# Optimization experiments

Hardware: AMD Instinct MI355X
Metric: run time of the kernel (lower is better)

## Reference

```python
import jax, jax.numpy as jnp
import numpy as np

B, L, D = 4, 2048, 1024
H, DK, DV = 16, 64, 64
TEMP = 8.0  # sqrt(DK)


def setup_inputs() -> dict:
    key = jax.random.key(0)
    ks = jax.random.split(key, 10)
    s = 0.02
    return {
        "q": jax.random.normal(ks[0], (B, L, D), jnp.float32),
        "k": jax.random.normal(ks[1], (B, L, D), jnp.float32),
        "v": jax.random.normal(ks[2], (B, L, D), jnp.float32),
        "mask": jax.random.randint(ks[3], (B, L, L), 0, 2).astype(jnp.int32),
        "Wq": jax.random.normal(ks[4], (D, H * DK), jnp.float32) * s,
        "bq": jnp.zeros((H * DK,), jnp.float32),
        "Wk": jax.random.normal(ks[5], (D, H * DK), jnp.float32) * s,
        "bk": jnp.zeros((H * DK,), jnp.float32),
        "Wv": jax.random.normal(ks[6], (D, H * DV), jnp.float32) * s,
        "bv": jnp.zeros((H * DV,), jnp.float32),
        "Wfc": jax.random.normal(ks[7], (H * DV, D), jnp.float32) * s,
        "bfc": jnp.zeros((D,), jnp.float32),
    }


def reference(q, k, v, mask, Wq, bq, Wk, bk, Wv, bv, Wfc, bfc):
    Bq, Lq, _ = q.shape
    res = q
    # QKV projections -> [B, H, L, dk/dv]
    qh = (q @ Wq + bq).reshape(Bq, Lq, H, DK).swapaxes(1, 2)
    kh = (k @ Wk + bk).reshape(Bq, k.shape[1], H, DK).swapaxes(1, 2)
    vh = (v @ Wv + bv).reshape(Bq, v.shape[1], H, DV).swapaxes(1, 2)
    # scaled scores [B, H, Lq, Lk]
    att = jnp.einsum("bhqd,bhkd->bhqk", qh / TEMP, kh)
    att = jnp.where(mask[:, None, :, :] == 0, jnp.float32(-1e9), att)
    att = jax.nn.softmax(att, axis=-1)
    # attend -> [B, H, Lq, dv] -> [B, Lq, H*dv]
    out = jnp.einsum("bhqk,bhkd->bhqd", att, vh)
    out = out.swapaxes(1, 2).reshape(Bq, Lq, H * DV)
    out = out @ Wfc + bfc + res  # dropout is identity in eval mode
    return (out, att)
```

## Files before the change

### kernel.cpp

```cpp
#include <hip/hip_runtime.h>
#include <cstddef>

namespace {

constexpr int B  = 4;
constexpr int L  = 2048;
constexpr int D  = 1024;
constexpr int H  = 16;
constexpr int DK = 64;
constexpr int HD = H * DK;
constexpr float INV_TEMP = 0.125f;
constexpr size_t NH = (size_t)B * H * L * DK;
constexpr int NROWS = B * H * L;
constexpr int NJT = L / 128;

typedef __bf16 bf16;
typedef bf16 bf16x4 __attribute__((ext_vector_type(4)));
typedef bf16 bf16x8 __attribute__((ext_vector_type(8)));
typedef float f32x4 __attribute__((ext_vector_type(4)));

__device__ __forceinline__ int swzc(int r, int c) {
    return c ^ (((r >> 3) & 7) << 2);
}

__global__ __launch_bounds__(256, 2)
void gemm_proj(const float* __restrict__ X, const float* __restrict__ W,
               const float* __restrict__ bias, bf16* __restrict__ outh,
               float scale, int vmode)
{
    __shared__ float As[128][64];
    __shared__ float Bs[64][128];
    const int tid = threadIdx.x;
    const int tx = tid & 15, ty = tid >> 4;
    const int m0 = blockIdx.x << 7;
    const int n0 = blockIdx.y << 7;
    float c[8][8] = {};

    for (int k0 = 0; k0 < D; k0 += 64) {
#pragma unroll
        for (int it = 0; it < 8; ++it) {
            const int idx = (it << 10) + (tid << 2);
            {
                const int r = idx >> 6, cb = idx & 63;
                *(float4*)&As[r][swzc(r, cb)] =
                    *(const float4*)(X + (size_t)(m0 + r) * D + k0 + cb);
            }
            {
                const int r = idx >> 7, cb = idx & 127;
                *(float4*)&Bs[r][cb] =
                    *(const float4*)(W + (size_t)(k0 + r) * HD + n0 + cb);
            }
        }
        __syncthreads();
        const int swA = (ty & 7) << 2;
#pragma unroll 2
        for (int kk = 0; kk < 64; kk += 4) {
            float4 a[8];
#pragma unroll
            for (int i = 0; i < 8; ++i)
                a[i] = *(const float4*)&As[(ty << 3) + i][kk ^ swA];
            float bl[4][4], bh_[4][4];
#pragma unroll
            for (int t = 0; t < 4; ++t) {
                const float4 b0 = *(const float4*)&Bs[kk + t][tx << 2];
                const float4 b1 = *(const float4*)&Bs[kk + t][(tx << 2) + 64];
                bl[t][0] = b0.x; bl[t][1] = b0.y; bl[t][2] = b0.z; bl[t][3] = b0.w;
                bh_[t][0] = b1.x; bh_[t][1] = b1.y; bh_[t][2] = b1.z; bh_[t][3] = b1.w;
            }
#pragma unroll
            for (int i = 0; i < 8; ++i) {
                const float af[4] = {a[i].x, a[i].y, a[i].z, a[i].w};
#pragma unroll
                for (int j = 0; j < 4; ++j) {
#pragma unroll
                    for (int t = 0; t < 4; ++t) {
                        c[i][j]     = fmaf(af[t], bl[t][j], c[i][j]);
                        c[i][j + 4] = fmaf(af[t], bh_[t][j], c[i][j + 4]);
                    }
                }
            }
        }
        __syncthreads();
    }

    if (vmode) {
        const int b  = m0 >> 11;
        const int l0 = (m0 & (L - 1)) + (ty << 3);
#pragma unroll
        for (int j = 0; j < 8; ++j) {
            const int col = n0 + (tx << 2) + ((j < 4) ? j : 60 + j);
            const float bj = bias[col];
            bf16x8 rv;
#pragma unroll
            for (int i = 0; i < 8; ++i)
                rv[i] = (bf16)((c[i][j] + bj) * scale);
            *(bf16x8*)(outh + ((size_t)(b * H + (col >> 6)) * 64 + (col & 63)) * L + l0) = rv;
        }
    } else {
        const int nlo = n0 + (tx << 2);
        const int nhi = nlo + 64;
        const float4 blo = *(const float4*)(bias + nlo);
        const float4 bhi = *(const float4*)(bias + nhi);
        const int hlo = nlo >> 6, hhi = nhi >> 6;
        const int dlo = nlo & 63, dhi = nhi & 63;
#pragma unroll
        for (int i = 0; i < 8; ++i) {
            const int m = m0 + (ty << 3) + i;
            const int b = m >> 11;
            const int l = m & (L - 1);
            bf16x4 r0, r1;
            r0[0] = (bf16)((c[i][0] + blo.x) * scale);
            r0[1] = (bf16)((c[i][1] + blo.y) * scale);
            r0[2] = (bf16)((c[i][2] + blo.z) * scale);
            r0[3] = (bf16)((c[i][3] + blo.w) * scale);
            r1[0] = (bf16)((c[i][4] + bhi.x) * scale);
            r1[1] = (bf16)((c[i][5] + bhi.y) * scale);
            r1[2] = (bf16)((c[i][6] + bhi.z) * scale);
            r1[3] = (bf16)((c[i][7] + bhi.w) * scale);
            *(bf16x4*)(outh + ((((size_t)b * H + hlo) * L + l) << 6) + dlo) = r0;
            *(bf16x4*)(outh + ((((size_t)b * H + hhi) * L + l) << 6) + dhi) = r1;
        }
    }
}

__global__ __launch_bounds__(256)
void scores_kernel(const bf16* __restrict__ Qh, const bf16* __restrict__ Kh,
                   const int* __restrict__ mask, float* __restrict__ att,
                   float* __restrict__ part)
{
    const int tid  = threadIdx.x;
    const int lane = tid & 63;
    const int w    = tid >> 6;
    const int lr   = lane & 15;
    const int lg   = lane >> 4;
    const int j0 = blockIdx.x << 7;
    const int q0 = blockIdx.y << 7;
    const int bh = blockIdx.z;
    const int b  = bh >> 4;
    const bf16* Qb = Qh + (size_t)bh * L * DK;
    const bf16* Kb = Kh + (size_t)bh * L * DK;
    const int qw = q0 + (w << 5);

    f32x4 acc[2][8];
#pragma unroll
    for (int qt = 0; qt < 2; ++qt)
#pragma unroll
        for (int jt = 0; jt < 8; ++jt)
            acc[qt][jt] = (f32x4){0.f, 0.f, 0.f, 0.f};

#pragma unroll
    for (int kc = 0; kc < 2; ++kc) {
        bf16x8 a[2], kb[8];
#pragma unroll
        for (int qt = 0; qt < 2; ++qt)
            a[qt] = *(const bf16x8*)(Qb + (size_t)(qw + (qt << 4) + lr) * DK + (kc << 5) + (lg << 3));
#pragma unroll
        for (int jt = 0; jt < 8; ++jt)
            kb[jt] = *(const bf16x8*)(Kb + (size_t)(j0 + (jt << 4) + lr) * DK + (kc << 5) + (lg << 3));
#pragma unroll
        for (int qt = 0; qt < 2; ++qt)
#pragma unroll
            for (int jt = 0; jt < 8; ++jt)
                acc[qt][jt] = __builtin_amdgcn_mfma_f32_16x16x32_bf16(
                    a[qt], kb[jt], acc[qt][jt], 0, 0, 0);
    }

#pragma unroll
    for (int qt = 0; qt < 2; ++qt)
#pragma unroll
        for (int r = 0; r < 4; ++r) {
            const int q = qw + (qt << 4) + (lg << 2) + r;
            const int* mrow = mask + ((size_t)b * L + q) * L + j0 + lr;
            float* arow = att + ((size_t)bh * L + q) * L + j0 + lr;
            float vals[8];
#pragma unroll
            for (int jt = 0; jt < 8; ++jt) {
                const float vv = mrow[jt << 4] ? acc[qt][jt][r] : -1e9f;
                vals[jt] = vv;
                arow[jt << 4] = vv;
            }
            float mx = vals[0];
#pragma unroll
            for (int jt = 1; jt < 8; ++jt) mx = fmaxf(mx, vals[jt]);
            mx = fmaxf(mx, __shfl_xor(mx, 1, 16));
            mx = fmaxf(mx, __shfl_xor(mx, 2, 16));
            mx = fmaxf(mx, __shfl_xor(mx, 4, 16));
            mx = fmaxf(mx, __shfl_xor(mx, 8, 16));
            float sm = 0.f;
#pragma unroll
            for (int jt = 0; jt < 8; ++jt) sm += __expf(vals[jt] - mx);
            sm += __shfl_xor(sm, 1, 16);
            sm += __shfl_xor(sm, 2, 16);
            sm += __shfl_xor(sm, 4, 16);
            sm += __shfl_xor(sm, 8, 16);
            if (lr == 0)
                *(float2*)(part + (((size_t)bh * L + q) * NJT + blockIdx.x) * 2) =
                    make_float2(mx, sm);
        }
}

__global__ __launch_bounds__(256)
void rowstats_kernel(const float* __restrict__ part, float* __restrict__ stats)
{
    const int gid = blockIdx.x * 256 + threadIdx.x;
    const int row = gid >> 4;
    const int t   = gid & 15;
    const float2 p = *(const float2*)(part + ((size_t)row * NJT + t) * 2);
    float M = p.x;
    M = fmaxf(M, __shfl_xor(M, 1, 16));
    M = fmaxf(M, __shfl_xor(M, 2, 16));
    M = fmaxf(M, __shfl_xor(M, 4, 16));
    M = fmaxf(M, __shfl_xor(M, 8, 16));
    float s = p.y * __expf(p.x - M);
    s += __shfl_xor(s, 1, 16);
    s += __shfl_xor(s, 2, 16);
    s += __shfl_xor(s, 4, 16);
    s += __shfl_xor(s, 8, 16);
    if (t == 0)
        *(float2*)(stats + (size_t)row * 2) = make_float2(M, 1.0f / s);
}

__global__ __launch_bounds__(256)
void attv_kernel(float* __restrict__ att, const bf16* __restrict__ Vt,
                 const float* __restrict__ stats, float* __restrict__ O)
{
    const int tid  = threadIdx.x;
    const int lane = tid & 63;
    const int w    = tid >> 6;
    const int lr   = lane & 15;
    const int lg   = lane >> 4;
    const int m0 = blockIdx.x << 7;
    const int bh = blockIdx.y;
    const int qw = m0 + (w << 5);
    float* Ab = att + (size_t)bh * L * L;
    const bf16* Vb = Vt + (size_t)bh * 64 * L;

    f32x4 acc[2][4];
#pragma unroll
    for (int qt = 0; qt < 2; ++qt)
#pragma unroll
        for (int dt = 0; dt < 4; ++dt)
            acc[qt][dt] = (f32x4){0.f, 0.f, 0.f, 0.f};

    float Mq[2], Iq[2];
#pragma unroll
    for (int qt = 0; qt < 2; ++qt) {
        const float2 s2 = *(const float2*)(stats + ((size_t)bh * L + qw + (qt << 4) + lr) * 2);
        Mq[qt] = s2.x; Iq[qt] = s2.y;
    }

    for (int k0 = 0; k0 < L; k0 += 32) {
        bf16x8 pa[2];
#pragma unroll
        for (int qt = 0; qt < 2; ++qt) {
            float* sp = Ab + (size_t)(qw + (qt << 4) + lr) * L + k0 + (lg << 3);
            const float4 s0 = *(const float4*)sp;
            const float4 s1 = *(const float4*)(sp + 4);
            const float M = Mq[qt], inv = Iq[qt];
            const float p0 = __expf(s0.x - M) * inv;
            const float p1 = __expf(s0.y - M) * inv;
            const float p2 = __expf(s0.z - M) * inv;
            const float p3 = __expf(s0.w - M) * inv;
            const float p4 = __expf(s1.x - M) * inv;
            const float p5 = __expf(s1.y - M) * inv;
            const float p6 = __expf(s1.z - M) * inv;
            const float p7 = __expf(s1.w - M) * inv;
            *(float4*)sp       = make_float4(p0, p1, p2, p3);
            *(float4*)(sp + 4) = make_float4(p4, p5, p6, p7);
            bf16x8 a;
            a[0] = (bf16)p0; a[1] = (bf16)p1; a[2] = (bf16)p2; a[3] = (bf16)p3;
            a[4] = (bf16)p4; a[5] = (bf16)p5; a[6] = (bf16)p6; a[7] = (bf16)p7;
            pa[qt] = a;
        }
        bf16x8 vb[4];
#pragma unroll
        for (int dt = 0; dt < 4; ++dt)
            vb[dt] = *(const bf16x8*)(Vb + (size_t)((dt << 4) + lr) * L + k0 + (lg << 3));
#pragma unroll
        for (int qt = 0; qt < 2; ++qt)
#pragma unroll
            for (int dt = 0; dt < 4; ++dt)
                acc[qt][dt] = __builtin_amdgcn_mfma_f32_16x16x32_bf16(
                    pa[qt], vb[dt], acc[qt][dt], 0, 0, 0);
    }

#pragma unroll
    for (int qt = 0; qt < 2; ++qt)
#pragma unroll
        for (int dt = 0; dt < 4; ++dt)
#pragma unroll
            for (int r = 0; r < 4; ++r) {
                const int row = qw + (qt << 4) + (lg << 2) + r;
                O[((size_t)bh * L + row) * 64 + (dt << 4) + lr] = acc[qt][dt][r];
            }
}

__global__ __launch_bounds__(256, 2)
void fc_kernel(const float* __restrict__ O, const float* __restrict__ Wfc,
               const float* __restrict__ bfc, const float* __restrict__ resid,
               float* __restrict__ out)
{
    __shared__ float As[128][64];
    __shared__ float Bs[64][128];
    const int tid = threadIdx.x;
    const int tx = tid & 15, ty = tid >> 4;
    const int m0 = blockIdx.x << 7;
    const int n0 = blockIdx.y << 7;
    float c[8][8] = {};

    for (int k0 = 0; k0 < HD; k0 += 64) {
        const int h = k0 >> 6;
#pragma unroll
        for (int it = 0; it < 8; ++it) {
            const int idx = (it << 10) + (tid << 2);
            {
                const int r = idx >> 6, cb = idx & 63;
                const int m = m0 + r;
                const int b = m >> 11, l = m & (L - 1);
                *(float4*)&As[r][swzc(r, cb)] =
                    *(const float4*)(O + ((((size_t)b * H + h) * L + l) << 6) + cb);
            }
            {
                const int r = idx >> 7, cb = idx & 127;
                *(float4*)&Bs[r][cb] =
                    *(const float4*)(Wfc + (size_t)(k0 + r) * D + n0 + cb);
            }
        }
        __syncthreads();
        const int swA = (ty & 7) << 2;
#pragma unroll 2
        for (int kk = 0; kk < 64; kk += 4) {
            float4 a[8];
#pragma unroll
            for (int i = 0; i < 8; ++i)
                a[i] = *(const float4*)&As[(ty << 3) + i][kk ^ swA];
            float bl[4][4], bh_[4][4];
#pragma unroll
            for (int t = 0; t < 4; ++t) {
                const float4 b0 = *(const float4*)&Bs[kk + t][tx << 2];
                const float4 b1 = *(const float4*)&Bs[kk + t][(tx << 2) + 64];
                bl[t][0] = b0.x; bl[t][1] = b0.y; bl[t][2] = b0.z; bl[t][3] = b0.w;
                bh_[t][0] = b1.x; bh_[t][1] = b1.y; bh_[t][2] = b1.z; bh_[t][3] = b1.w;
            }
#pragma unroll
            for (int i = 0; i < 8; ++i) {
                const float af[4] = {a[i].x, a[i].y, a[i].z, a[i].w};
#pragma unroll
                for (int j = 0; j < 4; ++j)
#pragma unroll
                    for (int t = 0; t < 4; ++t) {
                        c[i][j]     = fmaf(af[t], bl[t][j], c[i][j]);
                        c[i][j + 4] = fmaf(af[t], bh_[t][j], c[i][j + 4]);
                    }
            }
        }
        __syncthreads();
    }

    const int nlo = n0 + (tx << 2);
    const int nhi = nlo + 64;
    const float4 blo = *(const float4*)(bfc + nlo);
    const float4 bhi = *(const float4*)(bfc + nhi);
#pragma unroll
    for (int i = 0; i < 8; ++i) {
        const int m = m0 + (ty << 3) + i;
        const float4 q0v = *(const float4*)(resid + (size_t)m * D + nlo);
        const float4 q1v = *(const float4*)(resid + (size_t)m * D + nhi);
        float4 r0, r1;
        r0.x = c[i][0] + blo.x + q0v.x; r0.y = c[i][1] + blo.y + q0v.y;
        r0.z = c[i][2] + blo.z + q0v.z; r0.w = c[i][3] + blo.w + q0v.w;
        r1.x = c[i][4] + bhi.x + q1v.x; r1.y = c[i][5] + bhi.y + q1v.y;
        r1.z = c[i][6] + bhi.z + q1v.z; r1.w = c[i][7] + bhi.w + q1v.w;
        *(float4*)(out + (size_t)m * D + nlo) = r0;
        *(float4*)(out + (size_t)m * D + nhi) = r1;
    }
}

}

extern "C" void kernel_launch(void* const* d_in, const int* in_sizes, int n_in,
                              void* d_out, int out_size, void* d_ws, size_t ws_size,
                              hipStream_t stream)
{
    const float* q    = (const float*)d_in[0];
    const float* k    = (const float*)d_in[1];
    const float* v    = (const float*)d_in[2];
    const int*   mask = (const int*)d_in[3];
    const float* Wq   = (const float*)d_in[4];
    const float* bq   = (const float*)d_in[5];
    const float* Wk   = (const float*)d_in[6];
    const float* bk   = (const float*)d_in[7];
    const float* Wv   = (const float*)d_in[8];
    const float* bv   = (const float*)d_in[9];
    const float* Wfc  = (const float*)d_in[10];
    const float* bfc  = (const float*)d_in[11];

    float* out = (float*)d_out;
    float* att = out + (size_t)B * L * D;

    bf16* Qh = (bf16*)d_ws;
    bf16* Kh = Qh + NH;
    bf16* Vt = Kh + NH;
    float* O    = (float*)(Vt + NH);
    float* stats = O + NH;
    float* part  = out;

    const dim3 blk(256);

    gemm_proj<<<dim3(64, 8), blk, 0, stream>>>(q, Wq, bq, Qh, INV_TEMP, 0);
    gemm_proj<<<dim3(64, 8), blk, 0, stream>>>(k, Wk, bk, Kh, 1.0f, 0);
    gemm_proj<<<dim3(64, 8), blk, 0, stream>>>(v, Wv, bv, Vt, 1.0f, 1);

    scores_kernel<<<dim3(L / 128, L / 128, B * H), blk, 0, stream>>>(Qh, Kh, mask, att, part);
    rowstats_kernel<<<dim3(NROWS * 16 / 256), blk, 0, stream>>>(part, stats);
    attv_kernel<<<dim3(L / 128, B * H), blk, 0, stream>>>(att, Vt, stats, O);
    fc_kernel<<<dim3(64, 8), blk, 0, stream>>>(O, Wfc, bfc, q, out);
}
```

Baseline: 2.805 ms.

## Switch projections to bf16 MFMA and fuse attention into a two-pass kernel

Replaces the fp32 FMA projection GEMMs with bf16 MFMA GEMMs fed by new conversion kernels that cast X to bf16 and transpose-cast the weights. Replaces the scores, rowstats and attv kernels with one fused attention kernel. Its first pass recomputes QK^T for online max/sum statistics and its second pass recomputes the scores, writes the normalized probabilities and accumulates P·V. This removes the fp32 score write and read-back round trip and the separate reduction launch. In exchange it computes QK^T twice, reads the mask twice, and adds per-call conversion passes.

Measured after the change: 2.301 ms. 17.9% less time.

```diff
diff --git a/kernel.cpp b/kernel.cpp
--- a/kernel.cpp
+++ b/kernel.cpp
@@ -11,8 +11,6 @@
 constexpr int HD = H * DK;
 constexpr float INV_TEMP = 0.125f;
 constexpr size_t NH = (size_t)B * H * L * DK;
-constexpr int NROWS = B * H * L;
-constexpr int NJT = L / 128;
 
 typedef __bf16 bf16;
 typedef bf16 bf16x4 __attribute__((ext_vector_type(4)));
@@ -23,265 +21,251 @@
     return c ^ (((r >> 3) & 7) << 2);
 }
 
+__global__ __launch_bounds__(256)
+void convW_kernel(const float* __restrict__ W, bf16* __restrict__ Wt)
+{
+    __shared__ float t[64][65];
+    const int k0 = blockIdx.x << 6, n0 = blockIdx.y << 6;
+    const int c = threadIdx.x & 63, r4 = threadIdx.x >> 6;
+#pragma unroll
+    for (int it = 0; it < 16; ++it) {
+        const int r = (it << 2) + r4;
+        t[r][c] = W[(size_t)(k0 + r) * HD + n0 + c];
+    }
+    __syncthreads();
+#pragma unroll
+    for (int it = 0; it < 16; ++it) {
+        const int r = (it << 2) + r4;
+        Wt[(size_t)(n0 + r) * D + k0 + c] = (bf16)t[c][r];
+    }
+}
+
+__global__ __launch_bounds__(256)
+void convX_kernel(const float* __restrict__ X, bf16* __restrict__ Xb)
+{
+    const size_t i = ((size_t)blockIdx.x * 256 + threadIdx.x) << 2;
+    const float4 v = *(const float4*)(X + i);
+    bf16x4 o;
+    o[0] = (bf16)v.x; o[1] = (bf16)v.y; o[2] = (bf16)v.z; o[3] = (bf16)v.w;
+    *(bf16x4*)(Xb + i) = o;
+}
+
 __global__ __launch_bounds__(256, 2)
-void gemm_proj(const float* __restrict__ X, const float* __restrict__ W,
+void proj_mfma(const bf16* __restrict__ Xb, const bf16* __restrict__ Wt,
                const float* __restrict__ bias, bf16* __restrict__ outh,
                float scale, int vmode)
-{
-    __shared__ float As[128][64];
-    __shared__ float Bs[64][128];
-    const int tid = threadIdx.x;
-    const int tx = tid & 15, ty = tid >> 4;
-    const int m0 = blockIdx.x << 7;
-    const int n0 = blockIdx.y << 7;
-    float c[8][8] = {};
-
-    for (int k0 = 0; k0 < D; k0 += 64) {
-#pragma unroll
-        for (int it = 0; it < 8; ++it) {
-            const int idx = (it << 10) + (tid << 2);
-            {
-                const int r = idx >> 6, cb = idx & 63;
-                *(float4*)&As[r][swzc(r, cb)] =
-                    *(const float4*)(X + (size_t)(m0 + r) * D + k0 + cb);
-            }
-            {
-                const int r = idx >> 7, cb = idx & 127;
-                *(float4*)&Bs[r][cb] =
-                    *(const float4*)(W + (size_t)(k0 + r) * HD + n0 + cb);
-            }
-        }
-        __syncthreads();
-        const int swA = (ty & 7) << 2;
-#pragma unroll 2
-        for (int kk = 0; kk < 64; kk += 4) {
-            float4 a[8];
-#pragma unroll
-            for (int i = 0; i < 8; ++i)
-                a[i] = *(const float4*)&As[(ty << 3) + i][kk ^ swA];
-            float bl[4][4], bh_[4][4];
-#pragma unroll
-            for (int t = 0; t < 4; ++t) {
-                const float4 b0 = *(const float4*)&Bs[kk + t][tx << 2];
-                const float4 b1 = *(const float4*)&Bs[kk + t][(tx << 2) + 64];
-                bl[t][0] = b0.x; bl[t][1] = b0.y; bl[t][2] = b0.z; bl[t][3] = b0.w;
-                bh_[t][0] = b1.x; bh_[t][1] = b1.y; bh_[t][2] = b1.z; bh_[t][3] = b1.w;
-            }
-#pragma unroll
-            for (int i = 0; i < 8; ++i) {
-                const float af[4] = {a[i].x, a[i].y, a[i].z, a[i].w};
-#pragma unroll
-                for (int j = 0; j < 4; ++j) {
-#pragma unroll
-                    for (int t = 0; t < 4; ++t) {
-                        c[i][j]     = fmaf(af[t], bl[t][j], c[i][j]);
-                        c[i][j + 4] = fmaf(af[t], bh_[t][j], c[i][j + 4]);
-                    }
-                }
-            }
-        }
-        __syncthreads();
-    }
-
-    if (vmode) {
-        const int b  = m0 >> 11;
-        const int l0 = (m0 & (L - 1)) + (ty << 3);
-#pragma unroll
-        for (int j = 0; j < 8; ++j) {
-            const int col = n0 + (tx << 2) + ((j < 4) ? j : 60 + j);
-            const float bj = bias[col];
-            bf16x8 rv;
-#pragma unroll
-            for (int i = 0; i < 8; ++i)
-                rv[i] = (bf16)((c[i][j] + bj) * scale);
-            *(bf16x8*)(outh + ((size_t)(b * H + (col >> 6)) * 64 + (col & 63)) * L + l0) = rv;
-        }
-    } else {
-        const int nlo = n0 + (tx << 2);
-        const int nhi = nlo + 64;
-        const float4 blo = *(const float4*)(bias + nlo);
-        const float4 bhi = *(const float4*)(bias + nhi);
-        const int hlo = nlo >> 6, hhi = nhi >> 6;
-        const int dlo = nlo & 63, dhi = nhi & 63;
-#pragma unroll
-        for (int i = 0; i < 8; ++i) {
-            const int m = m0 + (ty << 3) + i;
-            const int b = m >> 11;
-            const int l = m & (L - 1);
-            bf16x4 r0, r1;
-            r0[0] = (bf16)((c[i][0] + blo.x) * scale);
-            r0[1] = (bf16)((c[i][1] + blo.y) * scale);
-            r0[2] = (bf16)((c[i][2] + blo.z) * scale);
-            r0[3] = (bf16)((c[i][3] + blo.w) * scale);
-            r1[0] = (bf16)((c[i][4] + bhi.x) * scale);
-            r1[1] = (bf16)((c[i][5] + bhi.y) * scale);
-            r1[2] = (bf16)((c[i][6] + bhi.z) * scale);
-            r1[3] = (bf16)((c[i][7] + bhi.w) * scale);
-            *(bf16x4*)(outh + ((((size_t)b * H + hlo) * L + l) << 6) + dlo) = r0;
-            *(bf16x4*)(outh + ((((size_t)b * H + hhi) * L + l) << 6) + dhi) = r1;
-        }
-    }
-}
-
-__global__ __launch_bounds__(256)
-void scores_kernel(const bf16* __restrict__ Qh, const bf16* __restrict__ Kh,
-                   const int* __restrict__ mask, float* __restrict__ att,
-                   float* __restrict__ part)
 {
     const int tid  = threadIdx.x;
     const int lane = tid & 63;
     const int w    = tid >> 6;
     const int lr   = lane & 15;
     const int lg   = lane >> 4;
-    const int j0 = blockIdx.x << 7;
-    const int q0 = blockIdx.y << 7;
-    const int bh = blockIdx.z;
-    const int b  = bh >> 4;
-    const bf16* Qb = Qh + (size_t)bh * L * DK;
-    const bf16* Kb = Kh + (size_t)bh * L * DK;
-    const int qw = q0 + (w << 5);
-
-    f32x4 acc[2][8];
-#pragma unroll
-    for (int qt = 0; qt < 2; ++qt)
-#pragma unroll
-        for (int jt = 0; jt < 8; ++jt)
-            acc[qt][jt] = (f32x4){0.f, 0.f, 0.f, 0.f};
-
-#pragma unroll
-    for (int kc = 0; kc < 2; ++kc) {
-        bf16x8 a[2], kb[8];
-#pragma unroll
-        for (int qt = 0; qt < 2; ++qt)
-            a[qt] = *(const bf16x8*)(Qb + (size_t)(qw + (qt << 4) + lr) * DK + (kc << 5) + (lg << 3));
-#pragma unroll
-        for (int jt = 0; jt < 8; ++jt)
-            kb[jt] = *(const bf16x8*)(Kb + (size_t)(j0 + (jt << 4) + lr) * DK + (kc << 5) + (lg << 3));
-#pragma unroll
-        for (int qt = 0; qt < 2; ++qt)
-#pragma unroll
-            for (int jt = 0; jt < 8; ++jt)
-                acc[qt][jt] = __builtin_amdgcn_mfma_f32_16x16x32_bf16(
-                    a[qt], kb[jt], acc[qt][jt], 0, 0, 0);
-    }
-
-#pragma unroll
-    for (int qt = 0; qt < 2; ++qt)
-#pragma unroll
-        for (int r = 0; r < 4; ++r) {
-            const int q = qw + (qt << 4) + (lg << 2) + r;
-            const int* mrow = mask + ((size_t)b * L + q) * L + j0 + lr;
-            float* arow = att + ((size_t)bh * L + q) * L + j0 + lr;
-            float vals[8];
-#pragma unroll
-            for (int jt = 0; jt < 8; ++jt) {
-                const float vv = mrow[jt << 4] ? acc[qt][jt][r] : -1e9f;
-                vals[jt] = vv;
-                arow[jt << 4] = vv;
-            }
-            float mx = vals[0];
-#pragma unroll
-            for (int jt = 1; jt < 8; ++jt) mx = fmaxf(mx, vals[jt]);
-            mx = fmaxf(mx, __shfl_xor(mx, 1, 16));
-            mx = fmaxf(mx, __shfl_xor(mx, 2, 16));
-            mx = fmaxf(mx, __shfl_xor(mx, 4, 16));
-            mx = fmaxf(mx, __shfl_xor(mx, 8, 16));
-            float sm = 0.f;
-#pragma unroll
-            for (int jt = 0; jt < 8; ++jt) sm += __expf(vals[jt] - mx);
-            sm += __shfl_xor(sm, 1, 16);
-            sm += __shfl_xor(sm, 2, 16);
-            sm += __shfl_xor(sm, 4, 16);
-            sm += __shfl_xor(sm, 8, 16);
-            if (lr == 0)
-                *(float2*)(part + (((size_t)bh * L + q) * NJT + blockIdx.x) * 2) =
-                    make_float2(mx, sm);
-        }
-}
-
-__global__ __launch_bounds__(256)
-void rowstats_kernel(const float* __restrict__ part, float* __restrict__ stats)
-{
-    const int gid = blockIdx.x * 256 + threadIdx.x;
-    const int row = gid >> 4;
-    const int t   = gid & 15;
-    const float2 p = *(const float2*)(part + ((size_t)row * NJT + t) * 2);
-    float M = p.x;
-    M = fmaxf(M, __shfl_xor(M, 1, 16));
-    M = fmaxf(M, __shfl_xor(M, 2, 16));
-    M = fmaxf(M, __shfl_xor(M, 4, 16));
-    M = fmaxf(M, __shfl_xor(M, 8, 16));
-    float s = p.y * __expf(p.x - M);
-    s += __shfl_xor(s, 1, 16);
-    s += __shfl_xor(s, 2, 16);
-    s += __shfl_xor(s, 4, 16);
-    s += __shfl_xor(s, 8, 16);
-    if (t == 0)
-        *(float2*)(stats + (size_t)row * 2) = make_float2(M, 1.0f / s);
-}
-
-__global__ __launch_bounds__(256)
-void attv_kernel(float* __restrict__ att, const bf16* __restrict__ Vt,
-                 const float* __restrict__ stats, float* __restrict__ O)
+    const int bid  = blockIdx.x;
+    const int m0   = (bid >> 4) << 7;
+    const int n0   = (bid & 15) << 6;
+    const int mw   = m0 + (w << 5);
+
+    f32x4 acc[2][4];
+#pragma unroll
+    for (int mt = 0; mt < 2; ++mt)
+#pragma unroll
+        for (int nt = 0; nt < 4; ++nt)
+            acc[mt][nt] = (f32x4){0.f, 0.f, 0.f, 0.f};
+
+    for (int k0 = 0; k0 < D; k0 += 32) {
+        bf16x8 xa[2], wb[4];
+#pragma unroll
+        for (int mt = 0; mt < 2; ++mt)
+            xa[mt] = *(const bf16x8*)(Xb + (size_t)(mw + (mt << 4) + lr) * D + k0 + (lg << 3));
+#pragma unroll
+        for (int nt = 0; nt < 4; ++nt)
+            wb[nt] = *(const bf16x8*)(Wt + (size_t)(n0 + (nt << 4) + lr) * D + k0 + (lg << 3));
+#pragma unroll
+        for (int mt = 0; mt < 2; ++mt)
+#pragma unroll
+            for (int nt = 0; nt < 4; ++nt)
+                acc[mt][nt] = __builtin_amdgcn_mfma_f32_16x16x32_bf16(
+                    xa[mt], wb[nt], acc[mt][nt], 0, 0, 0);
+    }
+
+#pragma unroll
+    for (int mt = 0; mt < 2; ++mt) {
+        const int mbase = mw + (mt << 4) + (lg << 2);
+        const int b     = mbase >> 11;
+        const int lbase = mbase & (L - 1);
+#pragma unroll
+        for (int nt = 0; nt < 4; ++nt) {
+            const int n = n0 + (nt << 4) + lr;
+            const int h = n >> 6, d = n & 63;
+            const float bj = bias[n];
+            if (vmode) {
+                bf16x4 vv;
+#pragma unroll
+                for (int r = 0; r < 4; ++r)
+                    vv[r] = (bf16)((acc[mt][nt][r] + bj) * scale);
+                *(bf16x4*)(outh + ((size_t)(b * H + h) * 64 + d) * L + lbase) = vv;
+            } else {
+#pragma unroll
+                for (int r = 0; r < 4; ++r)
+                    outh[(((size_t)(b * H + h) * L + lbase + r) << 6) + d] =
+                        (bf16)((acc[mt][nt][r] + bj) * scale);
+            }
+        }
+    }
+}
+
+__global__ __launch_bounds__(256, 2)
+void fused_attn(const bf16* __restrict__ Qh, const bf16* __restrict__ Kh,
+                const bf16* __restrict__ Vt, const int* __restrict__ mask,
+                float* __restrict__ att, float* __restrict__ O)
 {
     const int tid  = threadIdx.x;
     const int lane = tid & 63;
     const int w    = tid >> 6;
     const int lr   = lane & 15;
     const int lg   = lane >> 4;
-    const int m0 = blockIdx.x << 7;
-    const int bh = blockIdx.y;
-    const int qw = m0 + (w << 5);
-    float* Ab = att + (size_t)bh * L * L;
-    const bf16* Vb = Vt + (size_t)bh * 64 * L;
-
-    f32x4 acc[2][4];
+    const int q0   = blockIdx.x << 7;
+    const int bh   = blockIdx.y;
+    const int b    = bh >> 4;
+    const int qw   = q0 + (w << 5);
+    const bf16* Qb = Qh + (size_t)bh * L * DK;
+    const bf16* Kb = Kh + (size_t)bh * L * DK;
+    const bf16* Vb = Vt + (size_t)bh * DK * L;
+
+    bf16x8 qf[2][2];
+    const int* mrow[2];
+    float* arow[2];
+#pragma unroll
+    for (int qt = 0; qt < 2; ++qt) {
+        const int q = qw + (qt << 4) + lr;
+#pragma unroll
+        for (int kc = 0; kc < 2; ++kc)
+            qf[qt][kc] = *(const bf16x8*)(Qb + (size_t)q * DK + (kc << 5) + (lg << 3));
+        mrow[qt] = mask + ((size_t)b * L + q) * L;
+        arow[qt] = att + ((size_t)bh * L + q) * L;
+    }
+
+    float mloc[2] = {-1e9f, -1e9f}, sloc[2] = {0.f, 0.f};
+    for (int j0 = 0; j0 < L; j0 += 32) {
+        bf16x8 kf[2][2];
+#pragma unroll
+        for (int jt = 0; jt < 2; ++jt)
+#pragma unroll
+            for (int kc = 0; kc < 2; ++kc)
+                kf[jt][kc] = *(const bf16x8*)(Kb + (size_t)(j0 + (jt << 4) + lr) * DK + (kc << 5) + (lg << 3));
+        f32x4 st[2][2];
+#pragma unroll
+        for (int qt = 0; qt < 2; ++qt)
+#pragma unroll
+            for (int jt = 0; jt < 2; ++jt)
+                st[qt][jt] = (f32x4){0.f, 0.f, 0.f, 0.f};
+#pragma unroll
+        for (int kc = 0; kc < 2; ++kc)
+#pragma unroll
+            for (int qt = 0; qt < 2; ++qt)
+#pragma unroll
+                for (int jt = 0; jt < 2; ++jt)
+                    st[qt][jt] = __builtin_amdgcn_mfma_f32_16x16x32_bf16(
+                        kf[jt][kc], qf[qt][kc], st[qt][jt], 0, 0, 0);
+#pragma unroll
+        for (int qt = 0; qt < 2; ++qt) {
+            float v[8];
+            float cm = -1e9f;
+#pragma unroll
+            for (int jt = 0; jt < 2; ++jt)
+#pragma unroll
+                for (int r = 0; r < 4; ++r) {
+                    const int j = j0 + (jt << 4) + (lg << 2) + r;
+                    const float s = mrow[qt][j] ? st[qt][jt][r] : -1e9f;
+                    v[(jt << 2) + r] = s;
+                    cm = fmaxf(cm, s);
+                }
+            const float nm = fmaxf(mloc[qt], cm);
+            float s8 = 0.f;
+#pragma unroll
+            for (int e = 0; e < 8; ++e) s8 += __expf(v[e] - nm);
+            sloc[qt] = sloc[qt] * __expf(mloc[qt] - nm) + s8;
+            mloc[qt] = nm;
+        }
+    }
+
+    float M[2], inv[2];
+#pragma unroll
+    for (int qt = 0; qt < 2; ++qt) {
+        float m_ = mloc[qt], s_ = sloc[qt];
+#pragma unroll
+        for (int off = 16; off < 64; off <<= 1) {
+            const float mo = __shfl_xor(m_, off);
+            const float so = __shfl_xor(s_, off);
+            const float nm = fmaxf(m_, mo);
+            s_ = s_ * __expf(m_ - nm) + so * __expf(mo - nm);
+            m_ = nm;
+        }
+        M[qt] = m_;
+        inv[qt] = 1.0f / s_;
+    }
+
+    f32x4 pacc[2][4];
 #pragma unroll
     for (int qt = 0; qt < 2; ++qt)
 #pragma unroll
         for (int dt = 0; dt < 4; ++dt)
-            acc[qt][dt] = (f32x4){0.f, 0.f, 0.f, 0.f};
-
-    float Mq[2], Iq[2];
-#pragma unroll
-    for (int qt = 0; qt < 2; ++qt) {
-        const float2 s2 = *(const float2*)(stats + ((size_t)bh * L + qw + (qt << 4) + lr) * 2);
-        Mq[qt] = s2.x; Iq[qt] = s2.y;
-    }
-
-    for (int k0 = 0; k0 < L; k0 += 32) {
-        bf16x8 pa[2];
+            pacc[qt][dt] = (f32x4){0.f, 0.f, 0.f, 0.f};
+
+    for (int j0 = 0; j0 < L; j0 += 32) {
+        bf16x8 kf[2][2];
+#pragma unroll
+        for (int jt = 0; jt < 2; ++jt)
+#pragma unroll
+            for (int kc = 0; kc < 2; ++kc)
+                kf[jt][kc] = *(const bf16x8*)(Kb + (size_t)(j0 + (jt << 4) + lr) * DK + (kc << 5) + (lg << 3));
+        f32x4 st[2][2];
+#pragma unroll
+        for (int qt = 0; qt < 2; ++qt)
+#pragma unroll
+            for (int jt = 0; jt < 2; ++jt)
+                st[qt][jt] = (f32x4){0.f, 0.f, 0.f, 0.f};
+#pragma unroll
+        for (int kc = 0; kc < 2; ++kc)
+#pragma unroll
+            for (int qt = 0; qt < 2; ++qt)
+#pragma unroll
+                for (int jt = 0; jt < 2; ++jt)
+                    st[qt][jt] = __builtin_amdgcn_mfma_f32_16x16x32_bf16(
+                        kf[jt][kc], qf[qt][kc], st[qt][jt], 0, 0, 0);
+
+        bf16x8 pf[2];
 #pragma unroll
         for (int qt = 0; qt < 2; ++qt) {
-            float* sp = Ab + (size_t)(qw + (qt << 4) + lr) * L + k0 + (lg << 3);
-            const float4 s0 = *(const float4*)sp;
-            const float4 s1 = *(const float4*)(sp + 4);
-            const float M = Mq[qt], inv = Iq[qt];
-            const float p0 = __expf(s0.x - M) * inv;
-            const float p1 = __expf(s0.y - M) * inv;
-            const float p2 = __expf(s0.z - M) * inv;
-            const float p3 = __expf(s0.w - M) * inv;
-            const float p4 = __expf(s1.x - M) * inv;
-            const float p5 = __expf(s1.y - M) * inv;
-            const float p6 = __expf(s1.z - M) * inv;
-            const float p7 = __expf(s1.w - M) * inv;
-            *(float4*)sp       = make_float4(p0, p1, p2, p3);
-            *(float4*)(sp + 4) = make_float4(p4, p5, p6, p7);
-            bf16x8 a;
-            a[0] = (bf16)p0; a[1] = (bf16)p1; a[2] = (bf16)p2; a[3] = (bf16)p3;
-            a[4] = (bf16)p4; a[5] = (bf16)p5; a[6] = (bf16)p6; a[7] = (bf16)p7;
-            pa[qt] = a;
-        }
-        bf16x8 vb[4];
-#pragma unroll
-        for (int dt = 0; dt < 4; ++dt)
-            vb[dt] = *(const bf16x8*)(Vb + (size_t)((dt << 4) + lr) * L + k0 + (lg << 3));
+#pragma unroll
+            for (int jt = 0; jt < 2; ++jt)
+#pragma unroll
+                for (int r = 0; r < 4; ++r) {
+                    const int j = j0 + (jt << 4) + (lg << 2) + r;
+                    const float s = mrow[qt][j] ? st[qt][jt][r] : -1e9f;
+                    const float p = __expf(s - M[qt]) * inv[qt];
+                    arow[qt][j] = p;
+                    pf[qt][(jt << 2) + r] = (bf16)p;
+                }
+        }
+
+        bf16x8 vf[4];
+#pragma unroll
+        for (int dt = 0; dt < 4; ++dt) {
+            const bf16* vp = Vb + (size_t)((dt << 4) + lr) * L + j0 + (lg << 2);
+            const bf16x4 v0 = *(const bf16x4*)vp;
+            const bf16x4 v1 = *(const bf16x4*)(vp + 16);
+            bf16x8 t;
+            t[0] = v0[0]; t[1] = v0[1]; t[2] = v0[2]; t[3] = v0[3];
+            t[4] = v1[0]; t[5] = v1[1]; t[6] = v1[2]; t[7] = v1[3];
+            vf[dt] = t;
+        }
 #pragma unroll
         for (int qt = 0; qt < 2; ++qt)
 #pragma unroll
             for (int dt = 0; dt < 4; ++dt)
-                acc[qt][dt] = __builtin_amdgcn_mfma_f32_16x16x32_bf16(
-                    pa[qt], vb[dt], acc[qt][dt], 0, 0, 0);
+                pacc[qt][dt] = __builtin_amdgcn_mfma_f32_16x16x32_bf16(
+                    pf[qt], vf[dt], pacc[qt][dt], 0, 0, 0);
     }
 
 #pragma unroll
@@ -291,7 +275,7 @@
 #pragma unroll
             for (int r = 0; r < 4; ++r) {
                 const int row = qw + (qt << 4) + (lg << 2) + r;
-                O[((size_t)bh * L + row) * 64 + (dt << 4) + lr] = acc[qt][dt][r];
+                O[((size_t)bh * L + row) * 64 + (dt << 4) + lr] = pacc[qt][dt][r];
             }
 }
 
@@ -398,21 +382,32 @@
     float* out = (float*)d_out;
     float* att = out + (size_t)B * L * D;
 
-    bf16* Qh = (bf16*)d_ws;
-    bf16* Kh = Qh + NH;
-    bf16* Vt = Kh + NH;
-    float* O    = (float*)(Vt + NH);
-    float* stats = O + NH;
-    float* part  = out;
+    float* O  = (float*)d_ws;
+    bf16* Xb  = (bf16*)d_ws;
+    bf16* Wtq = Xb + NH;
+    bf16* Wtk = Wtq + (size_t)D * HD;
+    bf16* Wtv = Wtk + (size_t)D * HD;
+    bf16* Qh  = (bf16*)(O + NH);
+    bf16* Kh  = Qh + NH;
+    bf16* Vt  = Kh + NH;
 
     const dim3 blk(256);
-
-    gemm_proj<<<dim3(64, 8), blk, 0, stream>>>(q, Wq, bq, Qh, INV_TEMP, 0);
-    gemm_proj<<<dim3(64, 8), blk, 0, stream>>>(k, Wk, bk, Kh, 1.0f, 0);
-    gemm_proj<<<dim3(64, 8), blk, 0, stream>>>(v, Wv, bv, Vt, 1.0f, 1);
-
-    scores_kernel<<<dim3(L / 128, L / 128, B * H), blk, 0, stream>>>(Qh, Kh, mask, att, part);
-    rowstats_kernel<<<dim3(NROWS * 16 / 256), blk, 0, stream>>>(part, stats);
-    attv_kernel<<<dim3(L / 128, B * H), blk, 0, stream>>>(att, Vt, stats, O);
+    const dim3 gW(D / 64, HD / 64);
+    const int gX = (int)(NH / 4 / 256);
+    const int gP = 1024;
+
+    convW_kernel<<<gW, blk, 0, stream>>>(Wq, Wtq);
+    convW_kernel<<<gW, blk, 0, stream>>>(Wk, Wtk);
+    convW_kernel<<<gW, blk, 0, stream>>>(Wv, Wtv);
+
+    convX_kernel<<<gX, blk, 0, stream>>>(q, Xb);
+    proj_mfma<<<gP, blk, 0, stream>>>(Xb, Wtq, bq, Qh, INV_TEMP, 0);
+    convX_kernel<<<gX, blk, 0, stream>>>(k, Xb);
+    proj_mfma<<<gP, blk, 0, stream>>>(Xb, Wtk, bk, Kh, 1.0f, 0);
+    convX_kernel<<<gX, blk, 0, stream>>>(v, Xb);
+    proj_mfma<<<gP, blk, 0, stream>>>(Xb, Wtv, bv, Vt, 1.0f, 1);
+
+    fused_attn<<<dim3(L / 128, B * H), blk, 0, stream>>>(Qh, Kh, Vt, mask, att, O);
+
     fc_kernel<<<dim3(64, 8), blk, 0, stream>>>(O, Wfc, bfc, q, out);
 }
```
